# Performance work log

Hardware: AMD Instinct MI355X
Metric: run time of the kernel (lower is better)

Reference implementation:

```python
import jax, jax.numpy as jnp
import numpy as np

DECAY = 0.99
EPSILON = 1e-05
NUM_CODES = 4096
CODE_DIM = 64
B, S = 16, 4096


def setup_inputs() -> dict:
    key = jax.random.key(0)
    k1, k2, k3 = jax.random.split(key, 3)
    x = jax.random.normal(k1, (B, S, CODE_DIM), dtype=jnp.float32)
    codebook = jax.random.normal(k2, (NUM_CODES, CODE_DIM), dtype=jnp.float32)
    cluster_size = jnp.zeros((NUM_CODES,), dtype=jnp.float32)
    ema_w = jax.random.normal(k3, (NUM_CODES, CODE_DIM), dtype=jnp.float32)
    return {"x": x, "codebook": codebook, "cluster_size": cluster_size, "ema_w": ema_w}


def reference(x, codebook, cluster_size, ema_w):
    Bd, Sd, D = x.shape
    flat_x = x.reshape(-1, D)  # [N, D], N = B*S
    # Monotone in true cdist(p=2), so argmin is identical to torch.cdist(...).argmin.
    x_sq = jnp.sum(flat_x * flat_x, axis=-1, keepdims=True)          # [N, 1]
    c_sq = jnp.sum(codebook * codebook, axis=-1)                     # [K]
    d2 = x_sq - 2.0 * (flat_x @ codebook.T) + c_sq[None, :]          # [N, K]
    indices = jnp.argmin(d2, axis=-1)                                # [N] int
    quantized = jnp.take(codebook, indices, axis=0).reshape(Bd, Sd, D)
    # Training-path EMA update (one-hot scatter-accumulate, done via segment ops).
    batch_cluster = jax.ops.segment_sum(
        jnp.ones_like(indices, dtype=flat_x.dtype), indices, num_segments=NUM_CODES)
    embed_sum = jax.ops.segment_sum(flat_x, indices, num_segments=NUM_CODES)  # [K, D]
    new_cluster_size = DECAY * cluster_size + (1.0 - DECAY) * batch_cluster
    new_ema_w = DECAY * ema_w + (1.0 - DECAY) * embed_sum
    n = jnp.sum(new_cluster_size)
    smoothed = (new_cluster_size + EPSILON) / (n + NUM_CODES * EPSILON) * n
    new_codebook = new_ema_w / smoothed[:, None]
    return (quantized, indices.reshape(Bd, Sd), new_codebook, new_cluster_size, new_ema_w)
```

## Files before the change

### kernel.cpp

```cpp
#include <hip/hip_runtime.h>

#define NUM_CODES 4096
#define CODE_DIM  64
#define NPTS      65536
#define NTILES    (NUM_CODES / 16)
#define NSEG2     8
#define SEGTILES  (NTILES / NSEG2)
#define DECAYF    0.99f
#define EPSF      1e-5f
#define THRF      0.02f

typedef __attribute__((ext_vector_type(8))) short short8v;
typedef __attribute__((ext_vector_type(4))) float f32x4;
#define MFMA16 __builtin_amdgcn_mfma_f32_16x16x32_bf16

#define WS_BC   0
#define WS_ES   4096
#define WS_N    266240
#define WS_CNT  266241
#define WS_CSQ  266244
#define WS_CF   270340
#define WS_TOP2 532484

#define OUT_Q    0
#define OUT_IDX  4194304
#define OUT_CB   4259840
#define OUT_CS   4521984
#define OUT_EMA  4526080

__device__ __forceinline__ unsigned short f2bf(float f) {
    unsigned u = __float_as_uint(f);
    u += 0x7FFFu + ((u >> 16) & 1u);
    return (unsigned short)(u >> 16);
}
__device__ __forceinline__ float bf2f(unsigned short h) {
    return __uint_as_float(((unsigned)h) << 16);
}

__global__ __launch_bounds__(256) void prep_all(const float* __restrict__ cb,
                                                float* __restrict__ csq,
                                                short* __restrict__ cf) {
    int k = blockIdx.x * 256 + threadIdx.x;
    const float4* cp = (const float4*)(cb + (size_t)k * CODE_DIM);
    float rowf[64];
    float s0 = 0.f, s1 = 0.f, s2 = 0.f, s3 = 0.f;
#pragma unroll
    for (int j = 0; j < 16; ++j) {
        float4 v = cp[j];
        rowf[4*j] = v.x; rowf[4*j+1] = v.y; rowf[4*j+2] = v.z; rowf[4*j+3] = v.w;
        s0 = fmaf(v.x, v.x, s0);
        s1 = fmaf(v.y, v.y, s1);
        s2 = fmaf(v.z, v.z, s2);
        s3 = fmaf(v.w, v.w, s3);
    }
    csq[k] = (s0 + s1) + (s2 + s3);

    int ctile = k >> 4;
    int r     = k & 15;
#pragma unroll
    for (int h = 0; h < 2; ++h) {
#pragma unroll
        for (int g = 0; g < 4; ++g) {
            int lane = g * 16 + r;
            short8v H, L;
#pragma unroll
            for (int j = 0; j < 8; ++j) {
                float s = -2.0f * rowf[h * 32 + g * 8 + j];
                unsigned short hb = f2bf(s);
                H[j] = (short)hb;
                L[j] = (short)f2bf(s - bf2f(hb));
            }
            *(short8v*)(cf + ((size_t)(ctile * 4 + h) * 64 + lane) * 8)     = H;
            *(short8v*)(cf + ((size_t)(ctile * 4 + 2 + h) * 64 + lane) * 8) = L;
        }
    }
}

__global__ __launch_bounds__(256) void scan_mfma(const float* __restrict__ x,
                                                 const short* __restrict__ cf,
                                                 const float* __restrict__ csq,
                                                 float4* __restrict__ top2) {
    const int wid  = threadIdx.x >> 6;
    const int lane = threadIdx.x & 63;
    const int blk  = blockIdx.x;
    const int pw   = blk >> 1;
    const int seg  = (blk & 1) * 4 + wid;
    const int col  = lane & 15;
    const int grp  = lane >> 4;
    const int pbase = pw * 64;

    short8v xh[4][2], xl[4][2];
#pragma unroll
    for (int t = 0; t < 4; ++t) {
#pragma unroll
        for (int h = 0; h < 2; ++h) {
            const float* xp = x + (size_t)(pbase + t * 16 + col) * CODE_DIM + h * 32 + grp * 8;
            float4 v0 = *(const float4*)(xp);
            float4 v1 = *(const float4*)(xp + 4);
            float f[8] = {v0.x, v0.y, v0.z, v0.w, v1.x, v1.y, v1.z, v1.w};
            short8v H, L;
#pragma unroll
            for (int j = 0; j < 8; ++j) {
                unsigned short hb = f2bf(f[j]);
                H[j] = (short)hb;
                L[j] = (short)f2bf(f[j] - bf2f(hb));
            }
            xh[t][h] = H; xl[t][h] = L;
        }
    }

    float m1[4], m2[4];
    int   i1[4];
#pragma unroll
    for (int t = 0; t < 4; ++t) { m1[t] = 3e38f; m2[t] = 3e38f; i1[t] = 0; }

#define LOAD_TILE(CT, AF, CQ) do { \
    const short* p_ = cf + ((size_t)(CT) * 4 * 64 + lane) * 8; \
    AF[0] = *(const short8v*)(p_); \
    AF[1] = *(const short8v*)(p_ + 64 * 8); \
    AF[2] = *(const short8v*)(p_ + 2 * 64 * 8); \
    AF[3] = *(const short8v*)(p_ + 3 * 64 * 8); \
    CQ = *(const float4*)(csq + (CT) * 16 + grp * 4); } while(0)

#define COMPUTE_TILE(CT, AF, CQ) do { \
    const int cbase_ = (CT) * 16 + grp * 4; \
    _Pragma("unroll") \
    for (int t = 0; t < 4; ++t) { \
        f32x4 a; a[0] = CQ.x; a[1] = CQ.y; a[2] = CQ.z; a[3] = CQ.w; \
        a = MFMA16(AF[0], xh[t][0], a, 0, 0, 0); \
        a = MFMA16(AF[1], xh[t][1], a, 0, 0, 0); \
        a = MFMA16(AF[0], xl[t][0], a, 0, 0, 0); \
        a = MFMA16(AF[1], xl[t][1], a, 0, 0, 0); \
        a = MFMA16(AF[2], xh[t][0], a, 0, 0, 0); \
        a = MFMA16(AF[3], xh[t][1], a, 0, 0, 0); \
        _Pragma("unroll") \
        for (int r = 0; r < 4; ++r) { \
            float k_ = a[r]; \
            bool lt_ = k_ < m1[t]; \
            float nm2_ = __builtin_amdgcn_fmed3f(m1[t], m2[t], k_); \
            i1[t] = lt_ ? (cbase_ + r) : i1[t]; \
            m1[t] = fminf(m1[t], k_); \
            m2[t] = nm2_; \
        } \
    } } while(0)

    short8v A0[4], A1[4];
    float4 q0, q1;
    const int tb = seg * SEGTILES;
    LOAD_TILE(tb, A0, q0);
#pragma unroll 4
    for (int it = 0; it < SEGTILES / 2; ++it) {
        const int t0 = tb + 2 * it, t1 = t0 + 1;
        const int t2 = (2 * it + 2 < SEGTILES) ? t1 + 1 : tb;
        LOAD_TILE(t1, A1, q1);
        COMPUTE_TILE(t0, A0, q0);
        LOAD_TILE(t2, A0, q0);
        COMPUTE_TILE(t1, A1, q1);
    }
#undef LOAD_TILE
#undef COMPUTE_TILE

#pragma unroll
    for (int t = 0; t < 4; ++t) {
#pragma unroll
        for (int off = 16; off <= 32; off <<= 1) {
            float om1 = __shfl_xor(m1[t], off);
            int   oi1 = __shfl_xor(i1[t], off);
            float om2 = __shfl_xor(m2[t], off);
            float nm2 = fminf(fmaxf(m1[t], om1), fminf(m2[t], om2));
            bool take = (om1 < m1[t]) || (om1 == m1[t] && oi1 < i1[t]);
            i1[t] = take ? oi1 : i1[t];
            m1[t] = fminf(m1[t], om1);
            m2[t] = nm2;
        }
    }
    if (lane < 16) {
#pragma unroll
        for (int t = 0; t < 4; ++t) {
            top2[(size_t)(pbase + t * 16 + lane) * NSEG2 + seg] =
                make_float4(m1[t], __int_as_float(i1[t]), m2[t], 0.0f);
        }
    }
}

__global__ __launch_bounds__(256) void emit1(const float4* __restrict__ top2,
                                             float* __restrict__ idx_out,
                                             float* __restrict__ bc_acc,
                                             int* __restrict__ flagged,
                                             int* __restrict__ cnt) {
    const int p = blockIdx.x * 256 + threadIdx.x;
    const int lane = threadIdx.x & 63;
    const float4* tp = top2 + (size_t)p * NSEG2;
    float4 t0 = tp[0];
    float m1 = t0.x; int i1 = __float_as_int(t0.y); float m2 = t0.z;
#pragma unroll
    for (int s = 1; s < NSEG2; ++s) {
        float4 t = tp[s];
        float om1 = t.x; int oi1 = __float_as_int(t.y); float om2 = t.z;
        float nm2 = fminf(fmaxf(m1, om1), fminf(m2, om2));
        bool take = (om1 < m1) || (om1 == m1 && oi1 < i1);
        if (take) i1 = oi1;
        m1 = fminf(m1, om1);
        m2 = nm2;
    }
    bool certified = (m2 - m1 >= THRF);
    if (certified) {
        idx_out[p] = (float)i1;
        atomicAdd(&bc_acc[i1], 1.0f);
    }
    unsigned long long mask = __ballot(!certified);
    int nw = __popcll(mask);
    int base = 0;
    if (lane == 0 && nw) base = atomicAdd(cnt, nw);
    base = __shfl(base, 0);
    if (!certified) {
        int off = __popcll(mask & ((1ULL << lane) - 1ULL));
        flagged[base + off] = p;
    }
}

__global__ __launch_bounds__(64) void fallback_kernel(const float* __restrict__ x,
                                                      const float* __restrict__ cb,
                                                      const int* __restrict__ flagged,
                                                      const int* __restrict__ cnt,
                                                      float* __restrict__ idx_out,
                                                      float* __restrict__ bc_acc) {
    __shared__ float xs[CODE_DIM];
    const int lane = threadIdx.x;
    const int n = *cnt;
    for (int w = blockIdx.x; w < n; w += 1024) {
        const int p = flagged[w];
        xs[lane] = x[(size_t)p * CODE_DIM + lane];
        __syncthreads();
        float4 xv[16];
#pragma unroll
        for (int q = 0; q < 16; ++q) xv[q] = *(const float4*)(xs + q * 4);
        double best = 1e300; int bi = 0;
        for (int j = 0; j < 64; ++j) {
            const int c = lane + 64 * j;
            const float4* cp = (const float4*)(cb + (size_t)c * CODE_DIM);
            double a0 = 0.0, a1 = 0.0, a2 = 0.0, a3 = 0.0;
#pragma unroll
            for (int q = 0; q < 16; ++q) {
                float4 cv = cp[q];
                double d0 = (double)xv[q].x - (double)cv.x;
                double d1 = (double)xv[q].y - (double)cv.y;
                double d2 = (double)xv[q].z - (double)cv.z;
                double d3 = (double)xv[q].w - (double)cv.w;
                a0 = fma(d0, d0, a0);
                a1 = fma(d1, d1, a1);
                a2 = fma(d2, d2, a2);
                a3 = fma(d3, d3, a3);
            }
            double acc = (a0 + a1) + (a2 + a3);
            if (acc < best) { best = acc; bi = c; }
        }
#pragma unroll
        for (int off = 1; off < 64; off <<= 1) {
            double ob = __shfl_xor(best, off);
            int   obi = __shfl_xor(bi, off);
            if (ob < best || (ob == best && obi < bi)) { best = ob; bi = obi; }
        }
        if (lane == 0) {
            idx_out[p] = (float)bi;
            atomicAdd(&bc_acc[bi], 1.0f);
        }
        __syncthreads();
    }
}

__global__ __launch_bounds__(256) void emit2(const float* __restrict__ x,
                                             const float* __restrict__ cb,
                                             const float* __restrict__ idx_out,
                                             float* __restrict__ q_out,
                                             float* __restrict__ es_acc) {
    const int p    = blockIdx.x * 4 + (threadIdx.x >> 6);
    const int lane = threadIdx.x & 63;
    const int fin  = (int)idx_out[p];
    float xv = x[(size_t)p * CODE_DIM + lane];
    float cv = cb[(size_t)fin * CODE_DIM + lane];
    q_out[(size_t)p * CODE_DIM + lane] = cv;
    atomicAdd(&es_acc[(size_t)fin * CODE_DIM + lane], xv);
}

__global__ __launch_bounds__(256) void ncs_kernel(const float* __restrict__ cs_in,
                                                  const float* __restrict__ bc_acc,
                                                  float* __restrict__ cs_out,
                                                  float* __restrict__ n_acc) {
    int k = blockIdx.x * 256 + threadIdx.x;
    float v = DECAYF * cs_in[k] + (1.0f - DECAYF) * bc_acc[k];
    cs_out[k] = v;
    float s = v;
#pragma unroll
    for (int off = 32; off > 0; off >>= 1) s += __shfl_down(s, off);
    if ((threadIdx.x & 63) == 0) atomicAdd(n_acc, s);
}

__global__ __launch_bounds__(256) void finalize_kernel(const float* __restrict__ ema_in,
                                                       const float* __restrict__ es_acc,
                                                       const float* __restrict__ cs_out,
                                                       const float* __restrict__ n_acc,
                                                       float* __restrict__ ema_out,
                                                       float* __restrict__ cb_out) {
    int idx = blockIdx.x * 256 + threadIdx.x;
    int k   = idx >> 6;
    float n = *n_acc;
    float ncs = cs_out[k];
    float smoothed = (ncs + EPSF) / (n + (float)NUM_CODES * EPSF) * n;
    float ew = DECAYF * ema_in[idx] + (1.0f - DECAYF) * es_acc[idx];
    ema_out[idx] = ew;
    cb_out[idx]  = ew / smoothed;
}

extern "C" void kernel_launch(void* const* d_in, const int* in_sizes, int n_in,
                              void* d_out, int out_size, void* d_ws, size_t ws_size,
                              hipStream_t stream) {
    const float* x    = (const float*)d_in[0];
    const float* cb   = (const float*)d_in[1];
    const float* cs   = (const float*)d_in[2];
    const float* emaw = (const float*)d_in[3];
    float* out = (float*)d_out;
    float* ws  = (float*)d_ws;

    hipMemsetAsync(ws, 0, (size_t)(WS_CNT + 1) * sizeof(float), stream);

    prep_all<<<NUM_CODES / 256, 256, 0, stream>>>(cb, ws + WS_CSQ, (short*)(ws + WS_CF));

    scan_mfma<<<(NPTS / 64) * NSEG2 / 4, 256, 0, stream>>>(
        x, (const short*)(ws + WS_CF), ws + WS_CSQ, (float4*)(ws + WS_TOP2));

    emit1<<<NPTS / 256, 256, 0, stream>>>(
        (const float4*)(ws + WS_TOP2), out + OUT_IDX, ws + WS_BC,
        (int*)(ws + WS_CF), (int*)(ws + WS_CNT));

    fallback_kernel<<<1024, 64, 0, stream>>>(
        x, cb, (const int*)(ws + WS_CF), (const int*)(ws + WS_CNT),
        out + OUT_IDX, ws + WS_BC);

    emit2<<<NPTS / 4, 256, 0, stream>>>(
        x, cb, out + OUT_IDX, out + OUT_Q, ws + WS_ES);

    ncs_kernel<<<NUM_CODES / 256, 256, 0, stream>>>(
        cs, ws + WS_BC, out + OUT_CS, ws + WS_N);

    finalize_kernel<<<(NUM_CODES * CODE_DIM) / 256, 256, 0, stream>>>(
        emaw, ws + WS_ES, out + OUT_CS, ws + WS_N, out + OUT_EMA, out + OUT_CB);
}
```

Before: 333.0 us.

## Pack argmin index into distance bits and privatize EMA accumulators

The scan loop now encodes each candidate's local code index into the low 9 mantissa bits of a biased distance. A positive bias is added to the squared norms so that unsigned integer min/med3 ops can track the top-2 keys without separate index registers. Top-2 results move to a compact segment-major uint2 layout. Atomic accumulation of cluster counts and embed sums is spread over 8 private copies that finalize sums, which also absorbs the separate ncs kernel. The total n is computed analytically in an extra prep block, and prep is parallelized to 8 threads per code. In exchange, the truncated mantissa forces a looser certification threshold, so more points may go to the fallback path, and the memset now clears a much larger workspace.

Result: faster. 310.4 us (-6.8%).

```diff
diff --git a/kernel.cpp b/kernel.cpp
--- a/kernel.cpp
+++ b/kernel.cpp
@@ -6,21 +6,36 @@
 #define NTILES    (NUM_CODES / 16)
 #define NSEG2     8
 #define SEGTILES  (NTILES / NSEG2)
+#define NCOPY     8
 #define DECAYF    0.99f
 #define EPSF      1e-5f
-#define THRF      0.02f
+#define BIASF     512.0f
+#define THRF      0.0625f
 
 typedef __attribute__((ext_vector_type(8))) short short8v;
 typedef __attribute__((ext_vector_type(4))) float f32x4;
 #define MFMA16 __builtin_amdgcn_mfma_f32_16x16x32_bf16
 
+__device__ __forceinline__ unsigned med3u(unsigned a, unsigned b, unsigned c) {
+    unsigned d;
+    asm("v_med3_u32 %0, %1, %2, %3" : "=v"(d) : "v"(a), "v"(b), "v"(c));
+    return d;
+}
+__device__ __forceinline__ unsigned min3u(unsigned a, unsigned b, unsigned c) {
+    unsigned d;
+    asm("v_min3_u32 %0, %1, %2, %3" : "=v"(d) : "v"(a), "v"(b), "v"(c));
+    return d;
+}
+__device__ __forceinline__ unsigned minu(unsigned a, unsigned b) { return a < b ? a : b; }
+__device__ __forceinline__ unsigned maxu(unsigned a, unsigned b) { return a > b ? a : b; }
+
 #define WS_BC   0
-#define WS_ES   4096
-#define WS_N    266240
-#define WS_CNT  266241
-#define WS_CSQ  266244
-#define WS_CF   270340
-#define WS_TOP2 532484
+#define WS_ES   32768
+#define WS_N    2129920
+#define WS_CNT  2129921
+#define WS_CSQ  2129924
+#define WS_CF   2134020
+#define WS_TOP2 2396164
 
 #define OUT_Q    0
 #define OUT_IDX  4194304
@@ -38,48 +53,57 @@
 }
 
 __global__ __launch_bounds__(256) void prep_all(const float* __restrict__ cb,
+                                                const float* __restrict__ cs_in,
                                                 float* __restrict__ csq,
-                                                short* __restrict__ cf) {
-    int k = blockIdx.x * 256 + threadIdx.x;
-    const float4* cp = (const float4*)(cb + (size_t)k * CODE_DIM);
-    float rowf[64];
-    float s0 = 0.f, s1 = 0.f, s2 = 0.f, s3 = 0.f;
-#pragma unroll
-    for (int j = 0; j < 16; ++j) {
-        float4 v = cp[j];
-        rowf[4*j] = v.x; rowf[4*j+1] = v.y; rowf[4*j+2] = v.z; rowf[4*j+3] = v.w;
-        s0 = fmaf(v.x, v.x, s0);
-        s1 = fmaf(v.y, v.y, s1);
-        s2 = fmaf(v.z, v.z, s2);
-        s3 = fmaf(v.w, v.w, s3);
-    }
-    csq[k] = (s0 + s1) + (s2 + s3);
-
-    int ctile = k >> 4;
-    int r     = k & 15;
-#pragma unroll
-    for (int h = 0; h < 2; ++h) {
-#pragma unroll
-        for (int g = 0; g < 4; ++g) {
-            int lane = g * 16 + r;
-            short8v H, L;
-#pragma unroll
-            for (int j = 0; j < 8; ++j) {
-                float s = -2.0f * rowf[h * 32 + g * 8 + j];
-                unsigned short hb = f2bf(s);
-                H[j] = (short)hb;
-                L[j] = (short)f2bf(s - bf2f(hb));
-            }
-            *(short8v*)(cf + ((size_t)(ctile * 4 + h) * 64 + lane) * 8)     = H;
-            *(short8v*)(cf + ((size_t)(ctile * 4 + 2 + h) * 64 + lane) * 8) = L;
-        }
-    }
+                                                short* __restrict__ cf,
+                                                float* __restrict__ n_out) {
+    if (blockIdx.x == 128) {
+        __shared__ float ws4[4];
+        int tid = threadIdx.x;
+        float s = 0.f;
+#pragma unroll
+        for (int j = 0; j < 16; ++j) s += cs_in[tid + 256 * j];
+#pragma unroll
+        for (int off = 32; off > 0; off >>= 1) s += __shfl_down(s, off);
+        if ((tid & 63) == 0) ws4[tid >> 6] = s;
+        __syncthreads();
+        if (tid == 0)
+            n_out[0] = DECAYF * (ws4[0] + ws4[1] + ws4[2] + ws4[3])
+                     + (1.0f - DECAYF) * (float)NPTS;
+        return;
+    }
+    int t     = blockIdx.x * 256 + threadIdx.x;
+    int code  = t >> 3;
+    int chunk = t & 7;
+    int khalf = chunk >> 2;
+    int g     = chunk & 3;
+    const float* src = cb + (size_t)code * CODE_DIM + khalf * 32 + g * 8;
+    float4 v0 = *(const float4*)(src);
+    float4 v1 = *(const float4*)(src + 4);
+    float f[8] = {v0.x, v0.y, v0.z, v0.w, v1.x, v1.y, v1.z, v1.w};
+    float sq = 0.f;
+    short8v H, L;
+#pragma unroll
+    for (int j = 0; j < 8; ++j) {
+        sq = fmaf(f[j], f[j], sq);
+        float s = -2.0f * f[j];
+        unsigned short hb = f2bf(s);
+        H[j] = (short)hb;
+        L[j] = (short)f2bf(s - bf2f(hb));
+    }
+#pragma unroll
+    for (int off = 1; off < 8; off <<= 1) sq += __shfl_xor(sq, off);
+    if (chunk == 0) csq[code] = sq + BIASF;
+    int ctile = code >> 4;
+    int lane_in_frag = g * 16 + (code & 15);
+    *(short8v*)(cf + ((size_t)(ctile * 4 + khalf) * 64 + lane_in_frag) * 8)     = H;
+    *(short8v*)(cf + ((size_t)(ctile * 4 + 2 + khalf) * 64 + lane_in_frag) * 8) = L;
 }
 
 __global__ __launch_bounds__(256) void scan_mfma(const float* __restrict__ x,
                                                  const short* __restrict__ cf,
                                                  const float* __restrict__ csq,
-                                                 float4* __restrict__ top2) {
+                                                 uint2* __restrict__ top2) {
     const int wid  = threadIdx.x >> 6;
     const int lane = threadIdx.x & 63;
     const int blk  = blockIdx.x;
@@ -87,6 +111,7 @@
     const int seg  = (blk & 1) * 4 + wid;
     const int col  = lane & 15;
     const int grp  = lane >> 4;
+    const unsigned grpsh = (unsigned)(grp << 2);
     const int pbase = pw * 64;
 
     short8v xh[4][2], xl[4][2];
@@ -109,10 +134,9 @@
         }
     }
 
-    float m1[4], m2[4];
-    int   i1[4];
-#pragma unroll
-    for (int t = 0; t < 4; ++t) { m1[t] = 3e38f; m2[t] = 3e38f; i1[t] = 0; }
+    unsigned m1k[4], m2k[4];
+#pragma unroll
+    for (int t = 0; t < 4; ++t) { m1k[t] = 0xFFFFFFFFu; m2k[t] = 0xFFFFFFFFu; }
 
 #define LOAD_TILE(CT, AF, CQ) do { \
     const short* p_ = cf + ((size_t)(CT) * 4 * 64 + lane) * 8; \
@@ -120,13 +144,14 @@
     AF[1] = *(const short8v*)(p_ + 64 * 8); \
     AF[2] = *(const short8v*)(p_ + 2 * 64 * 8); \
     AF[3] = *(const short8v*)(p_ + 3 * 64 * 8); \
-    CQ = *(const float4*)(csq + (CT) * 16 + grp * 4); } while(0)
+    CQ = *(const f32x4*)(csq + (CT) * 16 + grp * 4); } while(0)
 
 #define COMPUTE_TILE(CT, AF, CQ) do { \
-    const int cbase_ = (CT) * 16 + grp * 4; \
+    const unsigned tb9_ = (unsigned)(((CT) - tb) << 4) | grpsh; \
+    unsigned idx_[4] = {tb9_, tb9_ | 1u, tb9_ | 2u, tb9_ | 3u}; \
     _Pragma("unroll") \
     for (int t = 0; t < 4; ++t) { \
-        f32x4 a; a[0] = CQ.x; a[1] = CQ.y; a[2] = CQ.z; a[3] = CQ.w; \
+        f32x4 a = CQ; \
         a = MFMA16(AF[0], xh[t][0], a, 0, 0, 0); \
         a = MFMA16(AF[1], xh[t][1], a, 0, 0, 0); \
         a = MFMA16(AF[0], xl[t][0], a, 0, 0, 0); \
@@ -135,17 +160,14 @@
         a = MFMA16(AF[3], xh[t][1], a, 0, 0, 0); \
         _Pragma("unroll") \
         for (int r = 0; r < 4; ++r) { \
-            float k_ = a[r]; \
-            bool lt_ = k_ < m1[t]; \
-            float nm2_ = __builtin_amdgcn_fmed3f(m1[t], m2[t], k_); \
-            i1[t] = lt_ ? (cbase_ + r) : i1[t]; \
-            m1[t] = fminf(m1[t], k_); \
-            m2[t] = nm2_; \
+            unsigned key = (__float_as_uint(a[r]) & 0xFFFFFE00u) | idx_[r]; \
+            m2k[t] = med3u(m1k[t], m2k[t], key); \
+            m1k[t] = minu(m1k[t], key); \
         } \
     } } while(0)
 
     short8v A0[4], A1[4];
-    float4 q0, q1;
+    f32x4 q0, q1;
     const int tb = seg * SEGTILES;
     LOAD_TILE(tb, A0, q0);
 #pragma unroll 4
@@ -164,49 +186,44 @@
     for (int t = 0; t < 4; ++t) {
 #pragma unroll
         for (int off = 16; off <= 32; off <<= 1) {
-            float om1 = __shfl_xor(m1[t], off);
-            int   oi1 = __shfl_xor(i1[t], off);
-            float om2 = __shfl_xor(m2[t], off);
-            float nm2 = fminf(fmaxf(m1[t], om1), fminf(m2[t], om2));
-            bool take = (om1 < m1[t]) || (om1 == m1[t] && oi1 < i1[t]);
-            i1[t] = take ? oi1 : i1[t];
-            m1[t] = fminf(m1[t], om1);
-            m2[t] = nm2;
+            unsigned o1 = __shfl_xor(m1k[t], off);
+            unsigned o2 = __shfl_xor(m2k[t], off);
+            m2k[t] = min3u(maxu(m1k[t], o1), m2k[t], o2);
+            m1k[t] = minu(m1k[t], o1);
         }
     }
     if (lane < 16) {
 #pragma unroll
-        for (int t = 0; t < 4; ++t) {
-            top2[(size_t)(pbase + t * 16 + lane) * NSEG2 + seg] =
-                make_float4(m1[t], __int_as_float(i1[t]), m2[t], 0.0f);
-        }
-    }
-}
-
-__global__ __launch_bounds__(256) void emit1(const float4* __restrict__ top2,
+        for (int t = 0; t < 4; ++t)
+            top2[(size_t)seg * NPTS + pbase + t * 16 + lane] = make_uint2(m1k[t], m2k[t]);
+    }
+}
+
+__global__ __launch_bounds__(256) void emit1(const uint2* __restrict__ top2,
                                              float* __restrict__ idx_out,
                                              float* __restrict__ bc_acc,
                                              int* __restrict__ flagged,
                                              int* __restrict__ cnt) {
     const int p = blockIdx.x * 256 + threadIdx.x;
     const int lane = threadIdx.x & 63;
-    const float4* tp = top2 + (size_t)p * NSEG2;
-    float4 t0 = tp[0];
-    float m1 = t0.x; int i1 = __float_as_int(t0.y); float m2 = t0.z;
-#pragma unroll
-    for (int s = 1; s < NSEG2; ++s) {
-        float4 t = tp[s];
-        float om1 = t.x; int oi1 = __float_as_int(t.y); float om2 = t.z;
-        float nm2 = fminf(fmaxf(m1, om1), fminf(m2, om2));
-        bool take = (om1 < m1) || (om1 == m1 && oi1 < i1);
-        if (take) i1 = oi1;
-        m1 = fminf(m1, om1);
-        m2 = nm2;
-    }
-    bool certified = (m2 - m1 >= THRF);
+    unsigned M1 = 0xFFFFFFFFu, M2 = 0xFFFFFFFFu;
+    int wseg = 0;
+#pragma unroll
+    for (int s = 0; s < NSEG2; ++s) {
+        uint2 t = top2[(size_t)s * NPTS + p];
+        M2 = min3u(maxu(M1, t.x), M2, t.y);
+        if (t.x < M1) wseg = s;
+        M1 = minu(M1, t.x);
+    }
+    float m1v = __uint_as_float(M1 & 0xFFFFFE00u);
+    float m2v = __uint_as_float(M2 & 0xFFFFFE00u);
+    unsigned bits = M1 & 0x1FFu;
+    int code = (wseg * SEGTILES + (int)(bits >> 4)) * 16 + (int)((bits >> 2) & 3u) * 4 + (int)(bits & 3u);
+
+    bool certified = (m2v - m1v >= THRF);
     if (certified) {
-        idx_out[p] = (float)i1;
-        atomicAdd(&bc_acc[i1], 1.0f);
+        idx_out[p] = (float)code;
+        atomicAdd(&bc_acc[(blockIdx.x & (NCOPY - 1)) * NUM_CODES + code], 1.0f);
     }
     unsigned long long mask = __ballot(!certified);
     int nw = __popcll(mask);
@@ -228,6 +245,7 @@
     __shared__ float xs[CODE_DIM];
     const int lane = threadIdx.x;
     const int n = *cnt;
+    float* bcc = bc_acc + (size_t)(blockIdx.x & (NCOPY - 1)) * NUM_CODES;
     for (int w = blockIdx.x; w < n; w += 1024) {
         const int p = flagged[w];
         xs[lane] = x[(size_t)p * CODE_DIM + lane];
@@ -263,7 +281,7 @@
         }
         if (lane == 0) {
             idx_out[p] = (float)bi;
-            atomicAdd(&bc_acc[bi], 1.0f);
+            atomicAdd(&bcc[bi], 1.0f);
         }
         __syncthreads();
     }
@@ -277,37 +295,34 @@
     const int p    = blockIdx.x * 4 + (threadIdx.x >> 6);
     const int lane = threadIdx.x & 63;
     const int fin  = (int)idx_out[p];
+    float* esc = es_acc + (size_t)(blockIdx.x & (NCOPY - 1)) * (NUM_CODES * CODE_DIM);
     float xv = x[(size_t)p * CODE_DIM + lane];
     float cv = cb[(size_t)fin * CODE_DIM + lane];
     q_out[(size_t)p * CODE_DIM + lane] = cv;
-    atomicAdd(&es_acc[(size_t)fin * CODE_DIM + lane], xv);
-}
-
-__global__ __launch_bounds__(256) void ncs_kernel(const float* __restrict__ cs_in,
-                                                  const float* __restrict__ bc_acc,
-                                                  float* __restrict__ cs_out,
-                                                  float* __restrict__ n_acc) {
-    int k = blockIdx.x * 256 + threadIdx.x;
-    float v = DECAYF * cs_in[k] + (1.0f - DECAYF) * bc_acc[k];
-    cs_out[k] = v;
-    float s = v;
-#pragma unroll
-    for (int off = 32; off > 0; off >>= 1) s += __shfl_down(s, off);
-    if ((threadIdx.x & 63) == 0) atomicAdd(n_acc, s);
-}
-
-__global__ __launch_bounds__(256) void finalize_kernel(const float* __restrict__ ema_in,
+    atomicAdd(&esc[(size_t)fin * CODE_DIM + lane], xv);
+}
+
+__global__ __launch_bounds__(256) void finalize_kernel(const float* __restrict__ cs_in,
+                                                       const float* __restrict__ ema_in,
+                                                       const float* __restrict__ bc_acc,
                                                        const float* __restrict__ es_acc,
-                                                       const float* __restrict__ cs_out,
-                                                       const float* __restrict__ n_acc,
+                                                       const float* __restrict__ n_ptr,
+                                                       float* __restrict__ cs_out,
                                                        float* __restrict__ ema_out,
                                                        float* __restrict__ cb_out) {
     int idx = blockIdx.x * 256 + threadIdx.x;
     int k   = idx >> 6;
-    float n = *n_acc;
-    float ncs = cs_out[k];
+    float bc = 0.f, es = 0.f;
+#pragma unroll
+    for (int c = 0; c < NCOPY; ++c) {
+        bc += bc_acc[(size_t)c * NUM_CODES + k];
+        es += es_acc[(size_t)c * (NUM_CODES * CODE_DIM) + idx];
+    }
+    float ncs = DECAYF * cs_in[k] + (1.0f - DECAYF) * bc;
+    if ((idx & 63) == 0) cs_out[k] = ncs;
+    float n = *n_ptr;
     float smoothed = (ncs + EPSF) / (n + (float)NUM_CODES * EPSF) * n;
-    float ew = DECAYF * ema_in[idx] + (1.0f - DECAYF) * es_acc[idx];
+    float ew = DECAYF * ema_in[idx] + (1.0f - DECAYF) * es;
     ema_out[idx] = ew;
     cb_out[idx]  = ew / smoothed;
 }
@@ -324,13 +339,13 @@
 
     hipMemsetAsync(ws, 0, (size_t)(WS_CNT + 1) * sizeof(float), stream);
 
-    prep_all<<<NUM_CODES / 256, 256, 0, stream>>>(cb, ws + WS_CSQ, (short*)(ws + WS_CF));
+    prep_all<<<129, 256, 0, stream>>>(cb, cs, ws + WS_CSQ, (short*)(ws + WS_CF), ws + WS_N);
 
     scan_mfma<<<(NPTS / 64) * NSEG2 / 4, 256, 0, stream>>>(
-        x, (const short*)(ws + WS_CF), ws + WS_CSQ, (float4*)(ws + WS_TOP2));
+        x, (const short*)(ws + WS_CF), ws + WS_CSQ, (uint2*)(ws + WS_TOP2));
 
     emit1<<<NPTS / 256, 256, 0, stream>>>(
-        (const float4*)(ws + WS_TOP2), out + OUT_IDX, ws + WS_BC,
+        (const uint2*)(ws + WS_TOP2), out + OUT_IDX, ws + WS_BC,
         (int*)(ws + WS_CF), (int*)(ws + WS_CNT));
 
     fallback_kernel<<<1024, 64, 0, stream>>>(
@@ -340,9 +355,7 @@
     emit2<<<NPTS / 4, 256, 0, stream>>>(
         x, cb, out + OUT_IDX, out + OUT_Q, ws + WS_ES);
 
-    ncs_kernel<<<NUM_CODES / 256, 256, 0, stream>>>(
-        cs, ws + WS_BC, out + OUT_CS, ws + WS_N);
-
     finalize_kernel<<<(NUM_CODES * CODE_DIM) / 256, 256, 0, stream>>>(
-        emaw, ws + WS_ES, out + OUT_CS, ws + WS_N, out + OUT_EMA, out + OUT_CB);
-}
+        cs, emaw, ws + WS_BC, ws + WS_ES, ws + WS_N,
+        out + OUT_CS, out + OUT_EMA, out + OUT_CB);
+}
```
